# Optimization experiments

Hardware: AMD Instinct MI355X
Metric: run time of the kernel (lower is better)

Reference implementation:

```python
import jax, jax.numpy as jnp
import numpy as np

N_NODES = 100000
N_EDGES = 600000
NUM_GRAPHS = 512
IN_DIM = 128
HID = 64
HEADS = 2
NEG_SLOPE = 0.2


def gat_layer(h_in, src, dst, W, a_s, a_d, b, n_nodes):
    # W: [F_in, H*C], a_s/a_d: [H, C], b: [H*C]
    H, C = a_s.shape
    h = (h_in @ W).reshape(n_nodes, H, C)            # [N,H,C]
    alpha_src = jnp.einsum('nhc,hc->nh', h, a_s)      # [N,H]
    alpha_dst = jnp.einsum('nhc,hc->nh', h, a_d)      # [N,H]
    e = alpha_src[src] + alpha_dst[dst]               # [E,H]
    e = jnp.where(e >= 0, e, NEG_SLOPE * e)           # leaky_relu
    # segment softmax over destination node
    m = jax.ops.segment_max(e, dst, num_segments=n_nodes)
    m = jnp.where(jnp.isfinite(m), m, 0.0)
    ex = jnp.exp(e - m[dst])                          # [E,H]
    denom = jax.ops.segment_sum(ex, dst, num_segments=n_nodes)
    alpha = ex / jnp.maximum(denom[dst], 1e-16)       # [E,H]
    out = jax.ops.segment_sum(alpha[:, :, None] * h[src], dst, num_segments=n_nodes)
    return out.reshape(n_nodes, H * C) + b


def setup_inputs() -> dict:
    key = jax.random.key(0)
    ks = jax.random.split(key, 16)
    x = jax.random.normal(ks[0], (N_NODES, IN_DIM), dtype=jnp.float32)
    edge_index = jax.random.randint(ks[1], (2, N_EDGES), 0, N_NODES, dtype=jnp.int32)
    batch = jnp.sort(jax.random.randint(ks[2], (N_NODES,), 0, NUM_GRAPHS, dtype=jnp.int32))
    s = lambda *d: 1.0 / np.sqrt(d[0])
    W1 = jax.random.normal(ks[3], (IN_DIM, HEADS * HID), jnp.float32) * s(IN_DIM)
    a_src1 = jax.random.normal(ks[4], (HEADS, HID), jnp.float32) * s(HID)
    a_dst1 = jax.random.normal(ks[5], (HEADS, HID), jnp.float32) * s(HID)
    b1 = jnp.zeros((HEADS * HID,), jnp.float32)
    W2 = jax.random.normal(ks[6], (HEADS * HID, HID), jnp.float32) * s(HEADS * HID)
    a_src2 = jax.random.normal(ks[7], (1, HID), jnp.float32) * s(HID)
    a_dst2 = jax.random.normal(ks[8], (1, HID), jnp.float32) * s(HID)
    b2 = jnp.zeros((HID,), jnp.float32)
    Wf1 = jax.random.normal(ks[9], (2 * HID, HID), jnp.float32) * s(2 * HID)
    bf1 = jnp.zeros((HID,), jnp.float32)
    Wf2 = jax.random.normal(ks[10], (HID, 1), jnp.float32) * s(HID)
    bf2 = jnp.zeros((1,), jnp.float32)
    return dict(x=x, edge_index=edge_index, batch=batch, W1=W1, a_src1=a_src1,
                a_dst1=a_dst1, b1=b1, W2=W2, a_src2=a_src2, a_dst2=a_dst2, b2=b2,
                Wf1=Wf1, bf1=bf1, Wf2=Wf2, bf2=bf2)


def reference(x, edge_index, batch, W1, a_src1, a_dst1, b1, W2, a_src2, a_dst2, b2,
              Wf1, bf1, Wf2, bf2):
    n = x.shape[0]
    loops = jnp.arange(n, dtype=edge_index.dtype)
    src = jnp.concatenate([edge_index[0], loops])
    dst = jnp.concatenate([edge_index[1], loops])
    h = gat_layer(x, src, dst, W1, a_src1, a_dst1, b1, n)
    h = jax.nn.relu(h)
    h = gat_layer(h, src, dst, W2, a_src2, a_dst2, b2, n)  # [N, HID]
    # global mean + max pool per graph
    ones = jnp.ones((n,), h.dtype)
    counts = jax.ops.segment_sum(ones, batch, num_segments=NUM_GRAPHS)  # [G]
    mean = jax.ops.segment_sum(h, batch, num_segments=NUM_GRAPHS) / jnp.maximum(counts, 1.0)[:, None]
    mx = jax.ops.segment_max(h, batch, num_segments=NUM_GRAPHS)
    mx = jnp.where(counts[:, None] > 0, mx, 0.0)
    pooled = jnp.concatenate([mean, mx], axis=1)  # [G, 2*HID]
    out = jax.nn.relu(pooled @ Wf1 + bf1) @ Wf2 + bf2  # [G, 1]
    return out
```

## Files before the change

### kernel.cpp

```cpp
#include <hip/hip_runtime.h>

#define N_NODESC 100000
#define N_EDGESC 600000
#define E_TOTC   700000
#define NUM_GRAPHSC 512
#define NEG_SLOPE 0.2f
#define NEG_INF_ENC 0x007FFFFFu
#define SCAN_NB 128

typedef unsigned short ushort_t;
typedef __attribute__((ext_vector_type(8))) short bf16x8;
typedef __attribute__((ext_vector_type(4))) float f32x4;

__device__ __forceinline__ unsigned enc_f32(float f) {
    unsigned u = __float_as_uint(f);
    return (u & 0x80000000u) ? ~u : (u | 0x80000000u);
}
__device__ __forceinline__ float dec_f32(unsigned u) {
    u = (u & 0x80000000u) ? (u ^ 0x80000000u) : ~u;
    return __uint_as_float(u);
}
__device__ __forceinline__ ushort_t f32_to_bf16(float f) {
    unsigned u = __float_as_uint(f);
    return (ushort_t)((u + 0x7FFFu + ((u >> 16) & 1u)) >> 16);
}
__device__ __forceinline__ float bf16_to_f32(ushort_t h) {
    return __uint_as_float(((unsigned)h) << 16);
}
__device__ __forceinline__ unsigned pack_bf16x2(float a, float b) {
    return (unsigned)f32_to_bf16(a) | ((unsigned)f32_to_bf16(b) << 16);
}

__device__ __forceinline__ void glds16(const void* g, void* l) {
    __builtin_amdgcn_global_load_lds(
        (const __attribute__((address_space(1))) void*)g,
        (__attribute__((address_space(3))) void*)l, 16, 0, 0);
}

__global__ __launch_bounds__(256) void init_all(float* __restrict__ msum,
                                                unsigned* __restrict__ mmax,
                                                float* __restrict__ cnt,
                                                int* __restrict__ deg,
                                                const float* __restrict__ W1,
                                                const float* __restrict__ W2,
                                                ushort_t* __restrict__ wPre1,
                                                ushort_t* __restrict__ wPre2) {
    int i = blockIdx.x * 256 + threadIdx.x;
    if (i < NUM_GRAPHSC * 64) { msum[i] = 0.f; mmax[i] = NEG_INF_ENC; }
    if (i < NUM_GRAPHSC) cnt[i] = 0.f;
    if (i < N_NODESC) deg[i] = 0;
    if (i < 128 * 128) {
        int n = i >> 7, k = i & 127;
        wPre1[n * 128 + k] = f32_to_bf16(W1[k * 128 + n]);
    } else if (i < 128 * 128 + 64 * 128) {
        int j = i - 128 * 128;
        int n = j >> 7, k = j & 127;
        wPre2[n * 128 + k] = f32_to_bf16(W2[k * 64 + n]);
    }
}

__global__ __launch_bounds__(256) void hist_dst(const int* __restrict__ ei,
                                                int* __restrict__ deg) {
    int e = blockIdx.x * blockDim.x + threadIdx.x;
    if (e >= E_TOTC) return;
    int d = (e < N_EDGESC) ? ei[N_EDGESC + e] : e - N_EDGESC;
    atomicAdd(&deg[d], 1);
}

__global__ __launch_bounds__(256) void scan_partial(const int* __restrict__ deg,
                                                    int* __restrict__ bsum, int n) {
    __shared__ int red[256];
    int chunk = (n + SCAN_NB - 1) / SCAN_NB;
    int lo = blockIdx.x * chunk, hi = min(lo + chunk, n);
    int s = 0;
    for (int i = lo + threadIdx.x; i < hi; i += 256) s += deg[i];
    red[threadIdx.x] = s;
    __syncthreads();
    for (int d = 128; d; d >>= 1) {
        if (threadIdx.x < d) red[threadIdx.x] += red[threadIdx.x + d];
        __syncthreads();
    }
    if (threadIdx.x == 0) bsum[blockIdx.x] = red[0];
}

__global__ __launch_bounds__(256) void scan_final(const int* __restrict__ deg,
                                                  const int* __restrict__ bsum,
                                                  int* __restrict__ off, int n) {
    __shared__ int bs[SCAN_NB];
    __shared__ int tile[256];
    __shared__ int carry;
    int t = threadIdx.x;
    if (t < SCAN_NB) bs[t] = bsum[t];
    __syncthreads();
    for (int d = 1; d < SCAN_NB; d <<= 1) {
        int v = (t >= d && t < SCAN_NB) ? bs[t - d] : 0;
        __syncthreads();
        if (t < SCAN_NB) bs[t] += v;
        __syncthreads();
    }
    if (t == 0) carry = blockIdx.x ? bs[blockIdx.x - 1] : 0;
    __syncthreads();
    int chunk = (n + SCAN_NB - 1) / SCAN_NB;
    int lo = blockIdx.x * chunk, hi = min(lo + chunk, n);
    for (int base = lo; base < hi; base += 256) {
        int i = base + t;
        int v = (i < hi) ? deg[i] : 0;
        tile[t] = v;
        __syncthreads();
        for (int d = 1; d < 256; d <<= 1) {
            int u = (t >= d) ? tile[t - d] : 0;
            __syncthreads();
            tile[t] += u;
            __syncthreads();
        }
        if (i < hi) off[i] = carry + tile[t] - v;
        __syncthreads();
        if (t == 0) carry += tile[255];
        __syncthreads();
    }
}

__global__ __launch_bounds__(256) void scatter_csr(const int* __restrict__ ei,
                                                   int* __restrict__ off,
                                                   int* __restrict__ csr) {
    int e = blockIdx.x * blockDim.x + threadIdx.x;
    if (e >= E_TOTC) return;
    int s, d;
    if (e < N_EDGESC) { s = ei[e]; d = ei[N_EDGESC + e]; } else { s = d = e - N_EDGESC; }
    int slot = atomicAdd(&off[d], 1);
    csr[slot] = s;
}

__global__ __launch_bounds__(64) void gemm1_mfma(const float* __restrict__ X,
                                                 const ushort_t* __restrict__ Wp,
                                                 const float* __restrict__ a_s,
                                                 const float* __restrict__ a_d,
                                                 float* __restrict__ as_out,
                                                 float* __restrict__ ad_out,
                                                 ushort_t* __restrict__ Y16, int N) {
    __shared__ float sx[2048];
    int lane = threadIdx.x;
    int quad = lane >> 4, l16 = lane & 15;
    size_t node0 = (size_t)blockIdx.x * 16;

    {
        int rhalf = lane >> 5;
        int cb = (lane & 31) * 16;
#pragma unroll
        for (int c = 0; c < 8; ++c) {
            int rl = 2 * c + rhalf;
            size_t grow = node0 + rl;
            if (grow >= (size_t)N) grow = N - 1;
            int goff = cb ^ ((rl & 15) << 4);
            glds16((const char*)(X + grow * 128) + goff,
                   (char*)sx + c * 1024);
        }
    }
    asm volatile("s_waitcnt vmcnt(0)" ::: "memory");
    __builtin_amdgcn_sched_barrier(0);

    const char* swx = (const char*)sx + l16 * 512;
    int skey = (l16 & 15) << 4;

    f32x4 acc[8];
#pragma unroll
    for (int ct = 0; ct < 8; ++ct) acc[ct] = (f32x4){0.f, 0.f, 0.f, 0.f};

#pragma unroll
    for (int kc = 0; kc < 4; ++kc) {
        int b = kc * 128 + quad * 32;
        float4 xa = *(const float4*)(swx + (b ^ skey));
        float4 xb = *(const float4*)(swx + ((b + 16) ^ skey));
        union { bf16x8 v; unsigned u[4]; } af;
        af.u[0] = pack_bf16x2(xa.x, xa.y);
        af.u[1] = pack_bf16x2(xa.z, xa.w);
        af.u[2] = pack_bf16x2(xb.x, xb.y);
        af.u[3] = pack_bf16x2(xb.z, xb.w);
#pragma unroll
        for (int ct = 0; ct < 8; ++ct) {
            bf16x8 bb = *(const bf16x8*)(Wp + (size_t)(ct * 16 + l16) * 128 + kc * 32 + quad * 8);
            acc[ct] = __builtin_amdgcn_mfma_f32_16x16x32_bf16(af.v, bb, acc[ct], 0, 0, 0);
        }
    }

    unsigned* Yu = (unsigned*)Y16;
    float asv0[4], asv1[4], adv0[4], adv1[4];
#pragma unroll
    for (int ct = 0; ct < 4; ++ct) {
        int c = ct * 16 + l16;
        asv0[ct] = a_s[c]; asv1[ct] = a_s[64 + c];
        adv0[ct] = a_d[c]; adv1[ct] = a_d[64 + c];
    }
#pragma unroll
    for (int r = 0; r < 4; ++r) {
        size_t row = node0 + quad * 4 + r;
        bool ok = row < (size_t)N;
        if (ok) {
#pragma unroll
            for (int ct = 0; ct < 4; ++ct)
                Yu[row * 64 + ct * 16 + l16] = pack_bf16x2(acc[ct][r], acc[ct + 4][r]);
        }
        float ps0 = 0.f, pd0 = 0.f, ps1 = 0.f, pd1 = 0.f;
#pragma unroll
        for (int ct = 0; ct < 4; ++ct) {
            ps0 += acc[ct][r] * asv0[ct];     pd0 += acc[ct][r] * adv0[ct];
            ps1 += acc[ct + 4][r] * asv1[ct]; pd1 += acc[ct + 4][r] * adv1[ct];
        }
#pragma unroll
        for (int sh = 1; sh < 16; sh <<= 1) {
            ps0 += __shfl_xor(ps0, sh); pd0 += __shfl_xor(pd0, sh);
            ps1 += __shfl_xor(ps1, sh); pd1 += __shfl_xor(pd1, sh);
        }
        if (l16 == 0 && ok) {
            *(float2*)(as_out + row * 2) = make_float2(ps0, ps1);
            *(float2*)(ad_out + row * 2) = make_float2(pd0, pd1);
        }
    }
}

__global__ __launch_bounds__(64) void gemm2_mfma(const ushort_t* __restrict__ Xb,
                                                 const ushort_t* __restrict__ Wp,
                                                 const float* __restrict__ a_s,
                                                 const float* __restrict__ a_d,
                                                 float* __restrict__ as_out,
                                                 float* __restrict__ ad_out,
                                                 ushort_t* __restrict__ Y16, int N) {
    __shared__ ushort_t sx[2048];
    int lane = threadIdx.x;
    int quad = lane >> 4, l16 = lane & 15;
    size_t node0 = (size_t)blockIdx.x * 16;

    {
        int rq = lane >> 4;
        int cb = (lane & 15) * 16;
#pragma unroll
        for (int c = 0; c < 4; ++c) {
            int rl = 4 * c + rq;
            size_t grow = node0 + rl;
            if (grow >= (size_t)N) grow = N - 1;
            int goff = cb ^ ((rl & 15) << 4);
            glds16((const char*)(Xb + grow * 128) + goff,
                   (char*)sx + c * 1024);
        }
    }
    asm volatile("s_waitcnt vmcnt(0)" ::: "memory");
    __builtin_amdgcn_sched_barrier(0);

    const char* swx = (const char*)sx + l16 * 256;
    int skey = (l16 & 15) << 4;

    f32x4 acc[4];
#pragma unroll
    for (int ct = 0; ct < 4; ++ct) acc[ct] = (f32x4){0.f, 0.f, 0.f, 0.f};

#pragma unroll
    for (int kc = 0; kc < 4; ++kc) {
        int b = kc * 64 + quad * 16;
        bf16x8 a = *(const bf16x8*)(swx + (b ^ skey));
#pragma unroll
        for (int ct = 0; ct < 4; ++ct) {
            bf16x8 bb = *(const bf16x8*)(Wp + (size_t)(ct * 16 + l16) * 128 + kc * 32 + quad * 8);
            acc[ct] = __builtin_amdgcn_mfma_f32_16x16x32_bf16(a, bb, acc[ct], 0, 0, 0);
        }
    }

    float asv[4], adv[4];
#pragma unroll
    for (int ct = 0; ct < 4; ++ct) { asv[ct] = a_s[ct * 16 + l16]; adv[ct] = a_d[ct * 16 + l16]; }
#pragma unroll
    for (int r = 0; r < 4; ++r) {
        size_t row = node0 + quad * 4 + r;
        bool ok = row < (size_t)N;
        if (ok) {
#pragma unroll
            for (int ct = 0; ct < 4; ++ct)
                Y16[row * 64 + ct * 16 + l16] = f32_to_bf16(acc[ct][r]);
        }
        float ps = acc[0][r] * asv[0] + acc[1][r] * asv[1] +
                   acc[2][r] * asv[2] + acc[3][r] * asv[3];
        float pd = acc[0][r] * adv[0] + acc[1][r] * adv[1] +
                   acc[2][r] * adv[2] + acc[3][r] * adv[3];
#pragma unroll
        for (int sh = 1; sh < 16; sh <<= 1) {
            ps += __shfl_xor(ps, sh);
            pd += __shfl_xor(pd, sh);
        }
        if (l16 == 0 && ok) { as_out[row] = ps; ad_out[row] = pd; }
    }
}

template <int H, bool RELU, bool OB16>
__global__ __launch_bounds__(256) void gat_gather(const int* __restrict__ off_end,
                                                  const int* __restrict__ deg,
                                                  const int* __restrict__ csr,
                                                  const float* __restrict__ as,
                                                  const float* __restrict__ ad,
                                                  const ushort_t* __restrict__ H16,
                                                  const float* __restrict__ b,
                                                  void* __restrict__ outp, int N) {
    int lane = threadIdx.x & 63;
    int wave = threadIdx.x >> 6;
    int l = lane & 15;
    int gbase = lane & 48;
    int n = blockIdx.x * 16 + wave * 4 + (lane >> 4);
    if (n >= N) return;
    int dg = deg[n];
    int o = off_end[n] - dg;
    float adv[H];
#pragma unroll
    for (int h = 0; h < H; ++h) adv[h] = ad[n * H + h];

    float acc[H][4], den[H];
#pragma unroll
    for (int h = 0; h < H; ++h) {
        den[h] = 0.f;
#pragma unroll
        for (int q = 0; q < 4; ++q) acc[h][q] = 0.f;
    }

    const unsigned* Hu = (const unsigned*)H16;

    for (int base = 0; base < dg; base += 16) {
        int i = base + l;
        bool valid = i < dg;
        int s = valid ? csr[o + i] : 0;
        float v[H];
        if (H == 2) {
            float2 p = valid ? ((const float2*)as)[s] : make_float2(0.f, 0.f);
            v[0] = p.x + adv[0];
            v[H - 1] = p.y + adv[H - 1];
        } else {
            v[0] = valid ? as[s] + adv[0] : 0.f;
        }
#pragma unroll
        for (int h = 0; h < H; ++h) {
            float e = v[h] >= 0.f ? v[h] : NEG_SLOPE * v[h];
            v[h] = valid ? __expf(e) : 0.f;
            den[h] += v[h];
        }
        int wpk = (H == 2) ? (int)pack_bf16x2(v[0], v[H - 1])
                           : (int)__float_as_uint(v[0]);
        int cnt = min(dg - base, 16);
        int cnt4 = (cnt + 3) & ~3;
        for (int j = 0; j < cnt4; j += 4) {
#pragma unroll
            for (int u = 0; u < 4; ++u) {
                int src = gbase + j + u;
                int sj = __shfl(s, src);
                int wp = __shfl(wpk, src);
                if (H == 2) {
                    float w0 = __uint_as_float(((unsigned)wp) << 16);
                    float w1 = __uint_as_float(((unsigned)wp) & 0xffff0000u);
                    uint4 hu = *(const uint4*)(Hu + (size_t)sj * 64 + l * 4);
                    acc[0][0] += w0 * __uint_as_float(hu.x << 16);
                    acc[H - 1][0] += w1 * __uint_as_float(hu.x & 0xffff0000u);
                    acc[0][1] += w0 * __uint_as_float(hu.y << 16);
                    acc[H - 1][1] += w1 * __uint_as_float(hu.y & 0xffff0000u);
                    acc[0][2] += w0 * __uint_as_float(hu.z << 16);
                    acc[H - 1][2] += w1 * __uint_as_float(hu.z & 0xffff0000u);
                    acc[0][3] += w0 * __uint_as_float(hu.w << 16);
                    acc[H - 1][3] += w1 * __uint_as_float(hu.w & 0xffff0000u);
                } else {
                    float w0 = __uint_as_float((unsigned)wp);
                    uint2 hu = *(const uint2*)((const unsigned*)(H16 + (size_t)sj * 64) + l * 2);
                    acc[0][0] += w0 * __uint_as_float(hu.x << 16);
                    acc[0][1] += w0 * __uint_as_float(hu.x & 0xffff0000u);
                    acc[0][2] += w0 * __uint_as_float(hu.y << 16);
                    acc[0][3] += w0 * __uint_as_float(hu.y & 0xffff0000u);
                }
            }
        }
    }
#pragma unroll
    for (int h = 0; h < H; ++h) {
#pragma unroll
        for (int sh = 8; sh; sh >>= 1) den[h] += __shfl_xor(den[h], sh);
    }
    if (H == 2) {
        float4 b0 = *(const float4*)(b + l * 4);
        float4 b1 = *(const float4*)(b + 64 + l * 4);
        float r0[4], r1[4];
        float id0 = 1.f / fmaxf(den[0], 1e-16f);
        float id1 = 1.f / fmaxf(den[H - 1], 1e-16f);
        r0[0] = acc[0][0] * id0 + b0.x; r0[1] = acc[0][1] * id0 + b0.y;
        r0[2] = acc[0][2] * id0 + b0.z; r0[3] = acc[0][3] * id0 + b0.w;
        r1[0] = acc[H - 1][0] * id1 + b1.x; r1[1] = acc[H - 1][1] * id1 + b1.y;
        r1[2] = acc[H - 1][2] * id1 + b1.z; r1[3] = acc[H - 1][3] * id1 + b1.w;
        if (RELU) {
#pragma unroll
            for (int q = 0; q < 4; ++q) { r0[q] = fmaxf(r0[q], 0.f); r1[q] = fmaxf(r1[q], 0.f); }
        }
        ushort_t* outb = (ushort_t*)outp;
        uint2 p0 = make_uint2(pack_bf16x2(r0[0], r0[1]), pack_bf16x2(r0[2], r0[3]));
        uint2 p1 = make_uint2(pack_bf16x2(r1[0], r1[1]), pack_bf16x2(r1[2], r1[3]));
        *(uint2*)(outb + (size_t)n * 128 + l * 4) = p0;
        *(uint2*)(outb + (size_t)n * 128 + 64 + l * 4) = p1;
    } else {
        float4 bv = *(const float4*)(b + l * 4);
        float id0 = 1.f / fmaxf(den[0], 1e-16f);
        float4 r;
        r.x = acc[0][0] * id0 + bv.x; r.y = acc[0][1] * id0 + bv.y;
        r.z = acc[0][2] * id0 + bv.z; r.w = acc[0][3] * id0 + bv.w;
        if (RELU) { r.x = fmaxf(r.x, 0.f); r.y = fmaxf(r.y, 0.f);
                    r.z = fmaxf(r.z, 0.f); r.w = fmaxf(r.w, 0.f); }
        *(float4*)((float*)outp + (size_t)n * 64 + l * 4) = r;
    }
}

__global__ __launch_bounds__(256) void pool_nodes(const float* __restrict__ h2,
                                                  const int* __restrict__ batch,
                                                  float* __restrict__ msum,
                                                  unsigned* __restrict__ mmax,
                                                  float* __restrict__ cnt, int N) {
    int wid = threadIdx.x >> 6, lane = threadIdx.x & 63;
    int n0 = (blockIdx.x * 4 + wid) * 64;
    if (n0 >= N) return;
    int n1 = min(n0 + 64, N);
    int curg = batch[n0];
    float s = 0.f, m = -1e30f;
    int c = 0;
    for (int n = n0; n < n1; ++n) {
        int g = batch[n];
        float v = h2[(size_t)n * 64 + lane];
        if (g != curg) {
            atomicAdd(&msum[curg * 64 + lane], s);
            atomicMax(&mmax[curg * 64 + lane], enc_f32(m));
            if (lane == 0) atomicAdd(&cnt[curg], (float)c);
            s = 0.f; m = -1e30f; c = 0; curg = g;
        }
        s += v;
        m = fmaxf(m, v);
        ++c;
    }
    atomicAdd(&msum[curg * 64 + lane], s);
    atomicMax(&mmax[curg * 64 + lane], enc_f32(m));
    if (lane == 0) atomicAdd(&cnt[curg], (float)c);
}

__global__ __launch_bounds__(64) void mlp_head(const float* __restrict__ msum,
                                               const unsigned* __restrict__ mmax,
                                               const float* __restrict__ cnt,
                                               const float* __restrict__ Wf1,
                                               const float* __restrict__ bf1,
                                               const float* __restrict__ Wf2,
                                               const float* __restrict__ bf2,
                                               float* __restrict__ out) {
    __shared__ float pooled[128];
    int g = blockIdx.x, lane = threadIdx.x;
    float c = cnt[g];
    pooled[lane] = msum[g * 64 + lane] / fmaxf(c, 1.0f);
    pooled[64 + lane] = (c > 0.f) ? dec_f32(mmax[g * 64 + lane]) : 0.f;
    __syncthreads();
    float acc = bf1[lane];
#pragma unroll
    for (int k = 0; k < 128; ++k) acc += pooled[k] * Wf1[k * 64 + lane];
    acc = fmaxf(acc, 0.f);
    float r = acc * Wf2[lane];
#pragma unroll
    for (int off = 32; off; off >>= 1) r += __shfl_xor(r, off);
    if (lane == 0) out[g] = r + bf2[0];
}

extern "C" void kernel_launch(void* const* d_in, const int* in_sizes, int n_in,
                              void* d_out, int out_size, void* d_ws, size_t ws_size,
                              hipStream_t stream) {
    const float* x    = (const float*)d_in[0];
    const int*   ei   = (const int*)d_in[1];
    const int*   batch= (const int*)d_in[2];
    const float* W1   = (const float*)d_in[3];
    const float* as1  = (const float*)d_in[4];
    const float* ad1  = (const float*)d_in[5];
    const float* b1   = (const float*)d_in[6];
    const float* W2   = (const float*)d_in[7];
    const float* as2  = (const float*)d_in[8];
    const float* ad2  = (const float*)d_in[9];
    const float* b2   = (const float*)d_in[10];
    const float* Wf1  = (const float*)d_in[11];
    const float* bf1  = (const float*)d_in[12];
    const float* Wf2  = (const float*)d_in[13];
    const float* bf2  = (const float*)d_in[14];
    float* out = (float*)d_out;

    const size_t N = N_NODESC;
    float* ws = (float*)d_ws;
    ushort_t* h16_1 = (ushort_t*)ws;
    ushort_t* out1b = (ushort_t*)(ws + N * 64);
    ushort_t* h16_2 = (ushort_t*)(ws + N * 128);
    float*    out2  = ws + N * 160;
    float*    small = ws + N * 224;
    float*    as1b = small;
    float*    ad1b = small + 2 * N;
    float*    as2b = small + 4 * N;
    float*    ad2b = small + 5 * N;
    float*    msum = small + 6 * N;
    unsigned* mmax = (unsigned*)(small + 6 * N + 512 * 64);
    float*    cntb = small + 6 * N + 2 * 512 * 64;
    int* ip  = (int*)(small + 6 * N + 2 * 512 * 64 + 512);
    int* deg  = ip;
    int* off  = ip + N;
    int* csr  = ip + 2 * N;
    int* bsum = ip + 2 * N + E_TOTC;
    ushort_t* wPre1 = (ushort_t*)(bsum + SCAN_NB);
    ushort_t* wPre2 = wPre1 + 128 * 128;

    init_all<<<(N_NODESC + 255) / 256, 256, 0, stream>>>(msum, mmax, cntb, deg,
                                                         W1, W2, wPre1, wPre2);

    hist_dst<<<(E_TOTC + 255) / 256, 256, 0, stream>>>(ei, deg);
    scan_partial<<<SCAN_NB, 256, 0, stream>>>(deg, bsum, N);
    scan_final<<<SCAN_NB, 256, 0, stream>>>(deg, bsum, off, N);
    scatter_csr<<<(E_TOTC + 255) / 256, 256, 0, stream>>>(ei, off, csr);

    const int NBLK16 = (N_NODESC + 15) / 16;

    gemm1_mfma<<<NBLK16, 64, 0, stream>>>(x, wPre1, as1, ad1, as1b, ad1b, h16_1, N);
    gat_gather<2, true, true><<<NBLK16, 256, 0, stream>>>(off, deg, csr, as1b,
                                                          ad1b, h16_1, b1, out1b, N);

    gemm2_mfma<<<NBLK16, 64, 0, stream>>>(out1b, wPre2, as2, ad2, as2b, ad2b, h16_2, N);
    gat_gather<1, false, false><<<NBLK16, 256, 0, stream>>>(off, deg, csr, as2b,
                                                            ad2b, h16_2, b2, out2, N);

    pool_nodes<<<(N + 255) / 256, 256, 0, stream>>>(out2, batch, msum, mmax, cntb, N);
    mlp_head<<<NUM_GRAPHSC, 64, 0, stream>>>(msum, mmax, cntb, Wf1, bf1, Wf2, bf2, out);
}
```

Before: 304.1 us.

## Fuse layer-2 projection GEMM into layer-1 attention gather epilogue

Removes the separate gemm2 kernel. The layer-1 gather kernel now writes its bf16 ReLU output into a swizzled shared-memory tile. Each of the block's four waves then runs MFMA for a 16-column slice of the layer-2 projection, and the block reduces the per-slice attention-score partials through shared memory. This avoids writing and re-reading the 128-wide layer-1 activations in global memory and saves one kernel launch. In exchange it adds shared memory, two block barriers sitting after an early return, and extra register pressure to the gather kernel, which could lower its occupancy.

```diff
diff --git a/kernel.cpp b/kernel.cpp
--- a/kernel.cpp
+++ b/kernel.cpp
@@ -218,78 +218,7 @@
     }
 }
 
-__global__ __launch_bounds__(64) void gemm2_mfma(const ushort_t* __restrict__ Xb,
-                                                 const ushort_t* __restrict__ Wp,
-                                                 const float* __restrict__ a_s,
-                                                 const float* __restrict__ a_d,
-                                                 float* __restrict__ as_out,
-                                                 float* __restrict__ ad_out,
-                                                 ushort_t* __restrict__ Y16, int N) {
-    __shared__ ushort_t sx[2048];
-    int lane = threadIdx.x;
-    int quad = lane >> 4, l16 = lane & 15;
-    size_t node0 = (size_t)blockIdx.x * 16;
-
-    {
-        int rq = lane >> 4;
-        int cb = (lane & 15) * 16;
-#pragma unroll
-        for (int c = 0; c < 4; ++c) {
-            int rl = 4 * c + rq;
-            size_t grow = node0 + rl;
-            if (grow >= (size_t)N) grow = N - 1;
-            int goff = cb ^ ((rl & 15) << 4);
-            glds16((const char*)(Xb + grow * 128) + goff,
-                   (char*)sx + c * 1024);
-        }
-    }
-    asm volatile("s_waitcnt vmcnt(0)" ::: "memory");
-    __builtin_amdgcn_sched_barrier(0);
-
-    const char* swx = (const char*)sx + l16 * 256;
-    int skey = (l16 & 15) << 4;
-
-    f32x4 acc[4];
-#pragma unroll
-    for (int ct = 0; ct < 4; ++ct) acc[ct] = (f32x4){0.f, 0.f, 0.f, 0.f};
-
-#pragma unroll
-    for (int kc = 0; kc < 4; ++kc) {
-        int b = kc * 64 + quad * 16;
-        bf16x8 a = *(const bf16x8*)(swx + (b ^ skey));
-#pragma unroll
-        for (int ct = 0; ct < 4; ++ct) {
-            bf16x8 bb = *(const bf16x8*)(Wp + (size_t)(ct * 16 + l16) * 128 + kc * 32 + quad * 8);
-            acc[ct] = __builtin_amdgcn_mfma_f32_16x16x32_bf16(a, bb, acc[ct], 0, 0, 0);
-        }
-    }
-
-    float asv[4], adv[4];
-#pragma unroll
-    for (int ct = 0; ct < 4; ++ct) { asv[ct] = a_s[ct * 16 + l16]; adv[ct] = a_d[ct * 16 + l16]; }
-#pragma unroll
-    for (int r = 0; r < 4; ++r) {
-        size_t row = node0 + quad * 4 + r;
-        bool ok = row < (size_t)N;
-        if (ok) {
-#pragma unroll
-            for (int ct = 0; ct < 4; ++ct)
-                Y16[row * 64 + ct * 16 + l16] = f32_to_bf16(acc[ct][r]);
-        }
-        float ps = acc[0][r] * asv[0] + acc[1][r] * asv[1] +
-                   acc[2][r] * asv[2] + acc[3][r] * asv[3];
-        float pd = acc[0][r] * adv[0] + acc[1][r] * adv[1] +
-                   acc[2][r] * adv[2] + acc[3][r] * adv[3];
-#pragma unroll
-        for (int sh = 1; sh < 16; sh <<= 1) {
-            ps += __shfl_xor(ps, sh);
-            pd += __shfl_xor(pd, sh);
-        }
-        if (l16 == 0 && ok) { as_out[row] = ps; ad_out[row] = pd; }
-    }
-}
-
-template <int H, bool RELU, bool OB16>
+template <int H, bool RELU, bool FUSE2>
 __global__ __launch_bounds__(256) void gat_gather(const int* __restrict__ off_end,
                                                   const int* __restrict__ deg,
                                                   const int* __restrict__ csr,
@@ -297,7 +226,17 @@
                                                   const float* __restrict__ ad,
                                                   const ushort_t* __restrict__ H16,
                                                   const float* __restrict__ b,
-                                                  void* __restrict__ outp, int N) {
+                                                  void* __restrict__ outp,
+                                                  const ushort_t* __restrict__ Wp2,
+                                                  const float* __restrict__ as2v,
+                                                  const float* __restrict__ ad2v,
+                                                  float* __restrict__ as2o,
+                                                  float* __restrict__ ad2o,
+                                                  ushort_t* __restrict__ h2out,
+                                                  int N) {
+    __shared__ char h1tile[16 * 256];
+    __shared__ float aspart[16][4];
+    __shared__ float adpart[16][4];
     int lane = threadIdx.x & 63;
     int wave = threadIdx.x >> 6;
     int l = lane & 15;
@@ -390,11 +329,18 @@
 #pragma unroll
             for (int q = 0; q < 4; ++q) { r0[q] = fmaxf(r0[q], 0.f); r1[q] = fmaxf(r1[q], 0.f); }
         }
-        ushort_t* outb = (ushort_t*)outp;
         uint2 p0 = make_uint2(pack_bf16x2(r0[0], r0[1]), pack_bf16x2(r0[2], r0[3]));
         uint2 p1 = make_uint2(pack_bf16x2(r1[0], r1[1]), pack_bf16x2(r1[2], r1[3]));
-        *(uint2*)(outb + (size_t)n * 128 + l * 4) = p0;
-        *(uint2*)(outb + (size_t)n * 128 + 64 + l * 4) = p1;
+        if (FUSE2) {
+            int g = threadIdx.x >> 4;
+            int key = (g & 15) << 4;
+            *(uint2*)(h1tile + g * 256 + ((l * 8) ^ key)) = p0;
+            *(uint2*)(h1tile + g * 256 + ((128 + l * 8) ^ key)) = p1;
+        } else {
+            ushort_t* outb = (ushort_t*)outp;
+            *(uint2*)(outb + (size_t)n * 128 + l * 4) = p0;
+            *(uint2*)(outb + (size_t)n * 128 + 64 + l * 4) = p1;
+        }
     } else {
         float4 bv = *(const float4*)(b + l * 4);
         float id0 = 1.f / fmaxf(den[0], 1e-16f);
@@ -404,6 +350,46 @@
         if (RELU) { r.x = fmaxf(r.x, 0.f); r.y = fmaxf(r.y, 0.f);
                     r.z = fmaxf(r.z, 0.f); r.w = fmaxf(r.w, 0.f); }
         *(float4*)((float*)outp + (size_t)n * 64 + l * 4) = r;
+    }
+
+    if (FUSE2) {
+        __syncthreads();
+        int quad = lane >> 4, l16 = lane & 15;
+        int skey = (l16 & 15) << 4;
+        const char* swx = h1tile + l16 * 256;
+        f32x4 acc2 = (f32x4){0.f, 0.f, 0.f, 0.f};
+#pragma unroll
+        for (int kc = 0; kc < 4; ++kc) {
+            int bb_ = kc * 64 + quad * 16;
+            bf16x8 a = *(const bf16x8*)(swx + (bb_ ^ skey));
+            bf16x8 bb = *(const bf16x8*)(Wp2 + (size_t)(wave * 16 + l16) * 128 + kc * 32 + quad * 8);
+            acc2 = __builtin_amdgcn_mfma_f32_16x16x32_bf16(a, bb, acc2, 0, 0, 0);
+        }
+        float asv = as2v[wave * 16 + l16], adv2 = ad2v[wave * 16 + l16];
+        size_t node0 = (size_t)blockIdx.x * 16;
+#pragma unroll
+        for (int r = 0; r < 4; ++r) {
+            size_t row = node0 + quad * 4 + r;
+            h2out[row * 64 + wave * 16 + l16] = f32_to_bf16(acc2[r]);
+            float ps = acc2[r] * asv, pd = acc2[r] * adv2;
+#pragma unroll
+            for (int sh = 1; sh < 16; sh <<= 1) {
+                ps += __shfl_xor(ps, sh);
+                pd += __shfl_xor(pd, sh);
+            }
+            if (l16 == 0) {
+                aspart[quad * 4 + r][wave] = ps;
+                adpart[quad * 4 + r][wave] = pd;
+            }
+        }
+        __syncthreads();
+        int t = threadIdx.x;
+        if (t < 16) {
+            as2o[node0 + t] = aspart[t][0] + aspart[t][1] + aspart[t][2] + aspart[t][3];
+        } else if (t < 32) {
+            int rr = t - 16;
+            ad2o[node0 + rr] = adpart[rr][0] + adpart[rr][1] + adpart[rr][2] + adpart[rr][3];
+        }
     }
 }
 
@@ -514,12 +500,13 @@
     const int NBLK16 = (N_NODESC + 15) / 16;
 
     gemm1_mfma<<<NBLK16, 64, 0, stream>>>(x, wPre1, as1, ad1, as1b, ad1b, h16_1, N);
-    gat_gather<2, true, true><<<NBLK16, 256, 0, stream>>>(off, deg, csr, as1b,
-                                                          ad1b, h16_1, b1, out1b, N);
-
-    gemm2_mfma<<<NBLK16, 64, 0, stream>>>(out1b, wPre2, as2, ad2, as2b, ad2b, h16_2, N);
-    gat_gather<1, false, false><<<NBLK16, 256, 0, stream>>>(off, deg, csr, as2b,
-                                                            ad2b, h16_2, b2, out2, N);
+    gat_gather<2, true, true><<<NBLK16, 256, 0, stream>>>(
+        off, deg, csr, as1b, ad1b, h16_1, b1, out1b,
+        wPre2, as2, ad2, as2b, ad2b, h16_2, N);
+
+    gat_gather<1, false, false><<<NBLK16, 256, 0, stream>>>(
+        off, deg, csr, as2b, ad2b, h16_2, b2, out2,
+        nullptr, nullptr, nullptr, nullptr, nullptr, nullptr, N);
 
     pool_nodes<<<(N + 255) / 256, 256, 0, stream>>>(out2, batch, msum, mmax, cntb, N);
     mlp_head<<<NUM_GRAPHSC, 64, 0, stream>>>(msum, mmax, cntb, Wf1, bf1, Wf2, bf2, out);
```

Result: faster. 293.4 us (-3.5%).
